# Performance work log

Hardware: AMD Instinct MI355X
Metric: run time of the kernel (lower is better)

The kernel has to match this reference:

```python
import jax, jax.numpy as jnp
import numpy as np

C = 256; Ca = C // 2; WH = 8; WW = 8; K = 3; NH = 8; HD = Ca // NH
EPS_LN = 1e-5; EPS_BN = 1e-5

def _rel_pos_idx(wh, ww):
    coords = np.stack(np.meshgrid(np.arange(wh), np.arange(ww), indexing='ij'))  # (2,wh,ww)
    flat = coords.reshape(2, -1)
    rel = (flat[:, :, None] - flat[:, None, :]).transpose(1, 2, 0).astype(np.int64)  # (N,N,2)
    rel[..., 0] += wh - 1
    rel[..., 1] += ww - 1
    rel[..., 0] *= 2 * ww - 1
    return jnp.asarray(rel.sum(-1))  # (N,N)

REL_IDX = _rel_pos_idx(WH, WW)

def _ln(x, g, b):
    m = x.mean(-1, keepdims=True)
    v = x.var(-1, keepdims=True)
    return (x - m) / jnp.sqrt(v + EPS_LN) * g + b

def _bn(x, g, b):  # eval-mode BN, running_mean=0, running_var=1; x is NCHW
    return x * (g / np.sqrt(1.0 + EPS_BN))[None, :, None, None] + b[None, :, None, None]

def _conv1x1(x, w, b):  # w: (O, I)
    return jnp.einsum('bchw,oc->bohw', x, w) + b[None, :, None, None]

def _rwp(x, h, w, wh, ww):  # windows (B*nW, wh*ww, c) -> image (B, c, h, w)
    Bn, N, c = x.shape
    nh, nw = h // wh, w // ww
    B = Bn // (nh * nw)
    x = x.reshape(B, nh, nw, wh, ww, c)
    return x.transpose(0, 5, 1, 3, 2, 4).reshape(B, c, h, w)

def _wp(x, wh, ww):  # image (B, c, h, w) -> windows (B*nW, wh*ww, c)
    B, c, h, w = x.shape
    x = x.reshape(B, c, h // wh, wh, w // ww, ww)
    return x.transpose(0, 2, 4, 3, 5, 1).reshape(-1, wh * ww, c)

def _gelu(t):
    return jax.nn.gelu(t, approximate=False)

def forward(x, rel_pos_bias, attn_w, attn_b, attn_ln_g, attn_ln_b,
            conv_w, conv_b, conv_bn_g, conv_bn_b,
            ci_w1, ci_b1, ci_bn_g, ci_bn_b, ci_w2, ci_b2,
            pr_w, pr_b, cn_bn_g, cn_bn_b,
            qkv_w, qkv_b,
            si_w1, si_b1, si_bn_g, si_bn_b, si_w2, si_b2,
            an_g, an_b, out_w, out_b, h, w):
    B_, N, Cfull = x.shape
    x_attn = _ln(x @ attn_w + attn_b, attn_ln_g, attn_ln_b)  # (B_, N, Ca)
    # conv branch -- note: source applies RWP to raw x (proj_cnn output is dead code)
    x_img = _rwp(x, h, w, WH, WW)  # (B, C, h, w)
    pad = K // 2
    x_cnn = jax.lax.conv_general_dilated(
        x_img, conv_w, (1, 1), [(pad, pad), (pad, pad)],
        dimension_numbers=('NCHW', 'OIHW', 'NCHW'), feature_group_count=Cfull)
    x_cnn = _gelu(_bn(x_cnn + conv_b[None, :, None, None], conv_bn_g, conv_bn_b))
    gap = x_cnn.mean((2, 3), keepdims=True)  # (B, C, 1, 1)
    ci = _conv1x1(gap, ci_w1, ci_b1)
    ci = _gelu(_bn(ci, ci_bn_g, ci_bn_b))
    ci = _conv1x1(ci, ci_w2, ci_b2)  # (B, Ca, 1, 1)
    x_cnn = _conv1x1(x_cnn, pr_w, pr_b)  # (B, Ca, h, w)
    # windowed attention
    qkv = (x_attn @ qkv_w + qkv_b).reshape(B_, N, 3, NH, HD).transpose(2, 0, 3, 1, 4)
    q, k, v = qkv[0], qkv[1], qkv[2]  # each (B_, NH, N, HD)
    B = ci.shape[0]
    ci_s = jax.nn.sigmoid(ci).reshape(B, 1, NH, 1, HD)
    v = (v.reshape(B, B_ // B, NH, N, HD) * ci_s).reshape(B_, NH, N, HD)
    scale = HD ** -0.5
    attn = jnp.einsum('bhnd,bhmd->bhnm', q * scale, k)
    bias = rel_pos_bias[REL_IDX]  # (N, N, NH)
    attn = jax.nn.softmax(attn + bias.transpose(2, 0, 1)[None], axis=-1)
    x_attn = jnp.einsum('bhnm,bhmd->bhnd', attn, v).transpose(0, 2, 1, 3).reshape(B_, N, Ca)
    # spatial interaction gating of conv branch
    x_sp = _rwp(x_attn, h, w, WH, WW)  # (B, Ca, h, w)
    si = _conv1x1(x_sp, si_w1, si_b1)
    si = _gelu(_bn(si, si_bn_g, si_bn_b))
    si = _conv1x1(si, si_w2, si_b2)  # (B, 1, h, w)
    x_cnn = jax.nn.sigmoid(si * x_cnn)
    x_cnn = _bn(x_cnn, cn_bn_g, cn_bn_b)
    x_cnn = _wp(x_cnn, WH, WW)  # (B_, N, Ca)
    x_attn = _ln(x_attn, an_g, an_b)
    return jnp.concatenate([x_attn, x_cnn], axis=-1) @ out_w + out_b

def setup_inputs() -> dict:
    key = jax.random.key(0)
    ks = jax.random.split(key, 12)
    B_, N = 2048, WH * WW
    s = 0.02
    return dict(
        x=jax.random.normal(ks[0], (B_, N, C), jnp.float32),
        rel_pos_bias=jax.random.uniform(ks[1], ((2 * WH - 1) * (2 * WW - 1), NH), jnp.float32),
        attn_w=jax.random.normal(ks[2], (C, Ca)) * s, attn_b=jnp.zeros((Ca,)),
        attn_ln_g=jnp.ones((Ca,)), attn_ln_b=jnp.zeros((Ca,)),
        conv_w=jax.random.normal(ks[3], (C, 1, K, K)) * s, conv_b=jnp.zeros((C,)),
        conv_bn_g=jnp.ones((C,)), conv_bn_b=jnp.zeros((C,)),
        ci_w1=jax.random.normal(ks[4], (C // 8, C)) * s, ci_b1=jnp.zeros((C // 8,)),
        ci_bn_g=jnp.ones((C // 8,)), ci_bn_b=jnp.zeros((C // 8,)),
        ci_w2=jax.random.normal(ks[5], (Ca, C // 8)) * s, ci_b2=jnp.zeros((Ca,)),
        pr_w=jax.random.normal(ks[6], (Ca, C)) * s, pr_b=jnp.zeros((Ca,)),
        cn_bn_g=jnp.ones((Ca,)), cn_bn_b=jnp.zeros((Ca,)),
        qkv_w=jax.random.normal(ks[7], (Ca, 3 * Ca)) * s, qkv_b=jnp.zeros((3 * Ca,)),
        si_w1=jax.random.normal(ks[8], (C // 16, Ca)) * s, si_b1=jnp.zeros((C // 16,)),
        si_bn_g=jnp.ones((C // 16,)), si_bn_b=jnp.zeros((C // 16,)),
        si_w2=jax.random.normal(ks[9], (1, C // 16)) * s, si_b2=jnp.zeros((1,)),
        an_g=jnp.ones((Ca,)), an_b=jnp.zeros((Ca,)),
        out_w=jax.random.normal(ks[10], (C, C)) * s, out_b=jnp.zeros((C,)),
        h=64, w=64,
    )

def reference(x, rel_pos_bias, attn_w, attn_b, attn_ln_g, attn_ln_b,
              conv_w, conv_b, conv_bn_g, conv_bn_b,
              ci_w1, ci_b1, ci_bn_g, ci_bn_b, ci_w2, ci_b2,
              pr_w, pr_b, cn_bn_g, cn_bn_b,
              qkv_w, qkv_b,
              si_w1, si_b1, si_bn_g, si_bn_b, si_w2, si_b2,
              an_g, an_b, out_w, out_b, h, w):
    return forward(x, rel_pos_bias, attn_w, attn_b, attn_ln_g, attn_ln_b,
                   conv_w, conv_b, conv_bn_g, conv_bn_b,
                   ci_w1, ci_b1, ci_bn_g, ci_bn_b, ci_w2, ci_b2,
                   pr_w, pr_b, cn_bn_g, cn_bn_b,
                   qkv_w, qkv_b,
                   si_w1, si_b1, si_bn_g, si_bn_b, si_w2, si_b2,
                   an_g, an_b, out_w, out_b, h, w)
```

## Files before the change

kernel.cpp:

```cpp
#include <hip/hip_runtime.h>
#include <math.h>


#define BNR 0.9999950000374998f
#define SQRT1_2 0.70710678118654752f

typedef __attribute__((ext_vector_type(8))) short short8;
typedef __attribute__((ext_vector_type(4))) float f32x4;
typedef __attribute__((ext_vector_type(4))) _Float16 half4;

__device__ __forceinline__ float gelu_f(float x) {
  return 0.5f * x * (1.0f + erff(x * SQRT1_2));
}
__device__ __forceinline__ unsigned short f2bf(float f) {
  unsigned int u = __builtin_bit_cast(unsigned int, f);
  u += 0x7fffu + ((u >> 16) & 1u);
  return (unsigned short)(u >> 16);
}
__device__ __forceinline__ float bf2f(unsigned short h) {
  unsigned int u = ((unsigned int)h) << 16;
  return __builtin_bit_cast(float, u);
}
__device__ __forceinline__ void ld8(const unsigned short* p, float* o) {
  const short8 v = *(const short8*)p;
#pragma unroll
  for (int i = 0; i < 8; ++i) o[i] = bf2f((unsigned short)v[i]);
}

#define ATI(r, ch) (((r) << 8) + ((((ch) ^ ((r)&7))) << 3))

__global__ __launch_bounds__(256) void kpack(
    const float* __restrict__ aw, const float* __restrict__ qw,
    const float* __restrict__ prw, const float* __restrict__ ow,
    const float* __restrict__ sw1, unsigned short* __restrict__ awp,
    unsigned short* __restrict__ qwp, unsigned short* __restrict__ prwp,
    unsigned short* __restrict__ owp, unsigned short* __restrict__ sw1p) {
  const int b = blockIdx.x;
  const float* src; unsigned short* dst; int fs, K, N, NT, trans;
  if (b < 64)       { fs = b;       src = aw;  dst = awp;  K = 256; N = 128; NT = 8;  trans = 0; }
  else if (b < 160) { fs = b - 64;  src = qw;  dst = qwp;  K = 128; N = 384; NT = 24; trans = 0; }
  else if (b < 224) { fs = b - 160; src = prw; dst = prwp; K = 256; N = 128; NT = 8;  trans = 1; }
  else if (b < 352) { fs = b - 224; src = ow;  dst = owp;  K = 256; N = 256; NT = 16; trans = 0; }
  else              { fs = b - 352; src = sw1; dst = sw1p; K = 128; N = 16;  NT = 1;  trans = 1; }
  const int ks = fs / NT, nt = fs % NT;
  for (int idx = threadIdx.x; idx < 512; idx += 256) {
    const int l = idx >> 3, i = idx & 7;
    const int k = ks * 32 + ((l >> 4) << 3) + i, n = nt * 16 + (l & 15);
    const float v = trans ? src[n * K + k] : src[k * N + n];
    dst[(fs * 64 + l) * 8 + i] = f2bf(v);
  }
}

__global__ __launch_bounds__(256) void k1_attn_ln(
    const float* __restrict__ x, const unsigned short* __restrict__ awp,
    const float* __restrict__ ab, const float* __restrict__ lg,
    const float* __restrict__ lb, unsigned short* __restrict__ xattn,
    unsigned short* __restrict__ xb) {
  const int tid = threadIdx.x, w = tid >> 6, l = tid & 63;
  const int lr = l & 15, lg4 = l >> 4;
  const int r0 = blockIdx.x * 64 + w * 16;
  const float* xp = x + (size_t)(r0 + lr) * 256 + lg4 * 8;
  unsigned short* xbp = xb + (size_t)(r0 + lr) * 256 + lg4 * 8;
  short8 a[8];
#pragma unroll
  for (int ks = 0; ks < 8; ++ks) {
    const float4 f0 = *(const float4*)(xp + ks * 32);
    const float4 f1 = *(const float4*)(xp + ks * 32 + 4);
    short8 av;
    av[0] = f2bf(f0.x); av[1] = f2bf(f0.y); av[2] = f2bf(f0.z); av[3] = f2bf(f0.w);
    av[4] = f2bf(f1.x); av[5] = f2bf(f1.y); av[6] = f2bf(f1.z); av[7] = f2bf(f1.w);
    a[ks] = av;
    *(short8*)(xbp + ks * 32) = av;
  }
  f32x4 acc[8];
#pragma unroll
  for (int nt = 0; nt < 8; ++nt) acc[nt] = (f32x4)0.f;
#pragma unroll
  for (int nt = 0; nt < 8; ++nt)
#pragma unroll
    for (int ks = 0; ks < 8; ++ks) {
      const short8 bfr = *(const short8*)(awp + ((ks * 8 + nt) * 64 + l) * 8);
      acc[nt] = __builtin_amdgcn_mfma_f32_16x16x32_bf16(a[ks], bfr, acc[nt], 0, 0, 0);
    }
  float bias[8], gam[8], bet[8];
#pragma unroll
  for (int nt = 0; nt < 8; ++nt) {
    const int col = nt * 16 + lr;
    bias[nt] = ab[col]; gam[nt] = lg[col]; bet[nt] = lb[col];
  }
#pragma unroll
  for (int j = 0; j < 4; ++j) {
    float s = 0.f, qq = 0.f;
#pragma unroll
    for (int nt = 0; nt < 8; ++nt) {
      const float v = acc[nt][j] + bias[nt];
      acc[nt][j] = v; s += v; qq += v * v;
    }
    s += __shfl_xor(s, 1); s += __shfl_xor(s, 2);
    s += __shfl_xor(s, 4); s += __shfl_xor(s, 8);
    qq += __shfl_xor(qq, 1); qq += __shfl_xor(qq, 2);
    qq += __shfl_xor(qq, 4); qq += __shfl_xor(qq, 8);
    const float mean = s * (1.f / 128.f);
    const float var = qq * (1.f / 128.f) - mean * mean;
    const float rstd = rsqrtf(var + 1e-5f);
    const int row = r0 + lg4 * 4 + j;
#pragma unroll
    for (int nt = 0; nt < 8; ++nt)
      xattn[(size_t)row * 128 + nt * 16 + lr] =
          f2bf((acc[nt][j] - mean) * rstd * gam[nt] + bet[nt]);
  }
}

__global__ __launch_bounds__(256) void k25_conv(
    const unsigned short* __restrict__ xb, const float* __restrict__ cw,
    const float* __restrict__ cb, const float* __restrict__ bg,
    const float* __restrict__ bb, const unsigned short* __restrict__ prwp,
    const float* __restrict__ prb, unsigned short* __restrict__ xpr,
    float* __restrict__ gpart) {
  __shared__ unsigned short gl[32][264];
  const int tid = threadIdx.x;
  const int b = blockIdx.x >> 7;
  const int y = (blockIdx.x >> 1) & 63;
  const int xt = (blockIdx.x & 1) * 32;
  const int w = tid >> 6, l = tid & 63;
  {
    const int c0 = l << 2;
    float4 w9[9];
#pragma unroll
    for (int k = 0; k < 9; ++k) {
      w9[k].x = cw[(c0 + 0) * 9 + k];
      w9[k].y = cw[(c0 + 1) * 9 + k];
      w9[k].z = cw[(c0 + 2) * 9 + k];
      w9[k].w = cw[(c0 + 3) * 9 + k];
    }
    const float4 cbv = *(const float4*)&cb[c0];
    float4 scv = *(const float4*)&bg[c0];
    scv.x *= BNR; scv.y *= BNR; scv.z *= BNR; scv.w *= BNR;
    const float4 sbv = *(const float4*)&bb[c0];
    float4 gsum = make_float4(0.f, 0.f, 0.f, 0.f);
    const int px0 = xt + w * 8;
#pragma unroll
    for (int sc2 = 0; sc2 < 2; ++sc2) {
      const int p0 = px0 + sc2 * 4;
      float4 v[3][6];
#pragma unroll
      for (int dy = 0; dy < 3; ++dy) {
        const int yy = y + dy - 1;
        const bool vy = (unsigned)yy < 64u;
        const int ybase = vy ? ((b * 64 + (yy >> 3) * 8) * 64 + (yy & 7) * 8) : 0;
#pragma unroll
        for (int q = 0; q < 6; ++q) {
          const int xx = p0 - 1 + q;
          float4 f = make_float4(0.f, 0.f, 0.f, 0.f);
          if (vy && (unsigned)xx < 64u) {
            const int row = ybase + (xx >> 3) * 64 + (xx & 7);
            const ushort4 u = *(const ushort4*)&xb[(size_t)row * 256 + c0];
            f.x = bf2f(u.x); f.y = bf2f(u.y); f.z = bf2f(u.z); f.w = bf2f(u.w);
          }
          v[dy][q] = f;
        }
      }
#pragma unroll
      for (int p = 0; p < 4; ++p) {
        float4 s = cbv;
#pragma unroll
        for (int dy = 0; dy < 3; ++dy)
#pragma unroll
          for (int dx = 0; dx < 3; ++dx) {
            const float wv_x = ((const float*)&w9[dy * 3 + dx])[0];
            const float4 wv = w9[dy * 3 + dx];
            const float4 vv = v[dy][p + dx];
            s.x = fmaf(wv.x, vv.x, s.x);
            s.y = fmaf(wv.y, vv.y, s.y);
            s.z = fmaf(wv.z, vv.z, s.z);
            s.w = fmaf(wv.w, vv.w, s.w);
            (void)wv_x;
          }
        s.x = s.x * scv.x + sbv.x; s.y = s.y * scv.y + sbv.y;
        s.z = s.z * scv.z + sbv.z; s.w = s.w * scv.w + sbv.w;
        const float g0 = gelu_f(s.x), g1 = gelu_f(s.y);
        const float g2 = gelu_f(s.z), g3 = gelu_f(s.w);
        ushort4 pk;
        pk.x = f2bf(g0); pk.y = f2bf(g1); pk.z = f2bf(g2); pk.w = f2bf(g3);
        *(ushort4*)&gl[w * 8 + sc2 * 4 + p][c0] = pk;
        gsum.x += g0; gsum.y += g1; gsum.z += g2; gsum.w += g3;
      }
    }
    *(float4*)&gpart[(size_t)blockIdx.x * 256 + c0] = gsum;
  }
  __syncthreads();
  const int lr = l & 15, lg4 = l >> 4;
  const int mr0 = (w & 1) * 16, nt0 = (w >> 1) * 4;
  short8 a[8];
#pragma unroll
  for (int ks = 0; ks < 8; ++ks)
    a[ks] = *(const short8*)&gl[mr0 + lr][ks * 32 + lg4 * 8];
  f32x4 acc[4];
#pragma unroll
  for (int nt = 0; nt < 4; ++nt) acc[nt] = (f32x4)0.f;
#pragma unroll
  for (int nt = 0; nt < 4; ++nt)
#pragma unroll
    for (int ks = 0; ks < 8; ++ks) {
      const short8 bfr =
          *(const short8*)(prwp + ((ks * 8 + nt0 + nt) * 64 + l) * 8);
      acc[nt] = __builtin_amdgcn_mfma_f32_16x16x32_bf16(a[ks], bfr, acc[nt], 0, 0, 0);
    }
#pragma unroll
  for (int nt = 0; nt < 4; ++nt) {
    const int col = (nt0 + nt) * 16 + lr;
    const float bv = prb[col];
#pragma unroll
    for (int j = 0; j < 4; ++j) {
      const int pix = (b * 64 + y) * 64 + xt + mr0 + lg4 * 4 + j;
      xpr[(size_t)pix * 128 + col] = f2bf(acc[nt][j] + bv);
    }
  }
}

__global__ __launch_bounds__(128) void k3_ci(
    const float* __restrict__ gp, const float* __restrict__ w1,
    const float* __restrict__ b1, const float* __restrict__ g1,
    const float* __restrict__ bb1, const float* __restrict__ w2,
    const float* __restrict__ b2, float* __restrict__ cis) {
  __shared__ float gm[256];
  __shared__ float c1[32];
  const int b = blockIdx.x, tid = threadIdx.x;
  for (int c = tid; c < 256; c += 128) {
    float s = 0.f;
    for (int p = 0; p < 128; ++p) s += gp[(size_t)(b * 128 + p) * 256 + c];
    gm[c] = s * (1.f / 4096.f);
  }
  __syncthreads();
  if (tid < 32) {
    float s = b1[tid];
    for (int c = 0; c < 256; ++c) s = fmaf(gm[c], w1[tid * 256 + c], s);
    s = s * (g1[tid] * BNR) + bb1[tid];
    c1[tid] = gelu_f(s);
  }
  __syncthreads();
  float s = b2[tid];
#pragma unroll
  for (int i = 0; i < 32; ++i) s = fmaf(c1[i], w2[tid * 32 + i], s);
  cis[b * 128 + tid] = 1.f / (1.f + __expf(-s));
}

__global__ __launch_bounds__(256) void k4_attn(
    const unsigned short* __restrict__ xa, const unsigned short* __restrict__ qwp,
    const float* __restrict__ qb, const float* __restrict__ cis,
    const float* __restrict__ rpb, unsigned short* __restrict__ attn) {
  __shared__ _Float16 Qs[64][130];
  __shared__ _Float16 Ks[64][130];
  __shared__ _Float16 VT[128][66];
  __shared__ float bsl[8][226];
  __shared__ float cisl[128];
  __shared__ float qbl[384];
  const int tid = threadIdx.x;
  const int win = blockIdx.x, img = win >> 6;
  for (int i = tid; i < 1800; i += 256) bsl[i & 7][i >> 3] = rpb[i];
  for (int i = tid; i < 128; i += 256) cisl[i] = cis[img * 128 + i];
  for (int i = tid; i < 384; i += 256) qbl[i] = qb[i];
  const int w = tid >> 6, l = tid & 63, lr = l & 15, lg4 = l >> 4;
  short8 a[4];
  const unsigned short* ap = xa + (size_t)(win * 64 + w * 16 + lr) * 128 + lg4 * 8;
#pragma unroll
  for (int ks = 0; ks < 4; ++ks) a[ks] = *(const short8*)(ap + ks * 32);
  f32x4 acc[24];
#pragma unroll
  for (int nt = 0; nt < 24; ++nt) acc[nt] = (f32x4)0.f;
#pragma unroll
  for (int nt = 0; nt < 24; ++nt)
#pragma unroll
    for (int ks = 0; ks < 4; ++ks) {
      const short8 bfr = *(const short8*)(qwp + ((ks * 24 + nt) * 64 + l) * 8);
      acc[nt] = __builtin_amdgcn_mfma_f32_16x16x32_bf16(a[ks], bfr, acc[nt], 0, 0, 0);
    }
  __syncthreads();
#pragma unroll
  for (int nt = 0; nt < 24; ++nt) {
    const int col = nt * 16 + lr;
#pragma unroll
    for (int j = 0; j < 4; ++j) {
      const int row = w * 16 + lg4 * 4 + j;
      const float v = acc[nt][j] + qbl[col];
      if (nt < 8) Qs[row][col] = (_Float16)(v * 0.25f);
      else if (nt < 16) Ks[row][col - 128] = (_Float16)v;
      else VT[col - 256][row] = (_Float16)(v * cisl[col - 256]);
    }
  }
  __syncthreads();
  for (int hi = 0; hi < 2; ++hi) {
    const int h = w * 2 + hi;
    half4 aK[4], bQ[4], bV[4];
#pragma unroll
    for (int mt = 0; mt < 4; ++mt)
      aK[mt] = *(const half4*)&Ks[mt * 16 + lr][h * 16 + lg4 * 4];
#pragma unroll
    for (int nt = 0; nt < 4; ++nt)
      bQ[nt] = *(const half4*)&Qs[nt * 16 + lr][h * 16 + lg4 * 4];
#pragma unroll
    for (int kt = 0; kt < 4; ++kt)
      bV[kt] = *(const half4*)&VT[h * 16 + lr][kt * 16 + lg4 * 4];
    f32x4 s[4][4];
#pragma unroll
    for (int mt = 0; mt < 4; ++mt)
#pragma unroll
      for (int nt = 0; nt < 4; ++nt)
        s[mt][nt] = __builtin_amdgcn_mfma_f32_16x16x16f16(aK[mt], bQ[nt],
                                                          (f32x4)0.f, 0, 0, 0);
#pragma unroll
    for (int mt = 0; mt < 4; ++mt) {
      const int m0 = mt * 16 + lg4 * 4;
#pragma unroll
      for (int r = 0; r < 4; ++r) {
        const int m = m0 + r;
        const int my = m >> 3, mxx = m & 7;
#pragma unroll
        for (int nt = 0; nt < 4; ++nt) {
          const int n = nt * 16 + lr;
          s[mt][nt][r] += bsl[h][((n >> 3) - my + 7) * 15 + (n & 7) - mxx + 7];
        }
      }
    }
    float inv[4];
#pragma unroll
    for (int nt = 0; nt < 4; ++nt) {
      float m0 = -1e30f;
#pragma unroll
      for (int mt = 0; mt < 4; ++mt)
#pragma unroll
        for (int r = 0; r < 4; ++r) m0 = fmaxf(m0, s[mt][nt][r]);
      m0 = fmaxf(m0, __shfl_xor(m0, 16));
      m0 = fmaxf(m0, __shfl_xor(m0, 32));
      float d0 = 0.f;
#pragma unroll
      for (int mt = 0; mt < 4; ++mt)
#pragma unroll
        for (int r = 0; r < 4; ++r) {
          const float e = __expf(s[mt][nt][r] - m0);
          s[mt][nt][r] = e;
          d0 += e;
        }
      d0 += __shfl_xor(d0, 16);
      d0 += __shfl_xor(d0, 32);
      inv[nt] = 1.f / d0;
    }
    half4 pa[4][4];
#pragma unroll
    for (int nt = 0; nt < 4; ++nt)
#pragma unroll
      for (int kt = 0; kt < 4; ++kt) {
        half4 p;
#pragma unroll
        for (int r = 0; r < 4; ++r) p[r] = (_Float16)(s[kt][nt][r] * inv[nt]);
        pa[nt][kt] = p;
      }
    f32x4 o[4];
#pragma unroll
    for (int nt = 0; nt < 4; ++nt) o[nt] = (f32x4)0.f;
#pragma unroll
    for (int nt = 0; nt < 4; ++nt)
#pragma unroll
      for (int kt = 0; kt < 4; ++kt)
        o[nt] = __builtin_amdgcn_mfma_f32_16x16x16f16(pa[nt][kt], bV[kt], o[nt], 0, 0, 0);
#pragma unroll
    for (int nt = 0; nt < 4; ++nt)
#pragma unroll
      for (int r = 0; r < 4; ++r) {
        const int token = win * 64 + nt * 16 + lg4 * 4 + r;
        attn[(size_t)token * 128 + h * 16 + lr] = f2bf(o[nt][r]);
      }
  }
}

__global__ __launch_bounds__(256) void k6_tail(
    const unsigned short* __restrict__ attn, const unsigned short* __restrict__ xpr,
    const unsigned short* __restrict__ sw1p, const float* __restrict__ sb1,
    const float* __restrict__ sgc, const float* __restrict__ sbc,
    const float* __restrict__ sw2, const float* __restrict__ sb2,
    const float* __restrict__ cg, const float* __restrict__ cbb,
    const float* __restrict__ ag, const float* __restrict__ abb,
    const unsigned short* __restrict__ owp, const float* __restrict__ ob,
    float* __restrict__ out) {
  __shared__ unsigned short At[64 * 256];
  __shared__ float sifl[64];
  __shared__ float statl[64][2];
  const int tid = threadIdx.x;
  const int R0 = blockIdx.x * 64;
  const int w = tid >> 6, l = tid & 63, lr = l & 15, lg4 = l >> 4;
  for (int i = tid; i < 1024; i += 256) {
    const int r = i >> 4, c16 = i & 15;
    *(uint4*)&At[ATI(r, c16)] =
        *(const uint4*)&attn[(size_t)(R0 + r) * 128 + c16 * 8];
    const int R = R0 + r, win = R >> 6, tt = R & 63;
    const int bimg = win >> 6, wy = (win >> 3) & 7, wx = win & 7;
    const int pix = (bimg * 64 + wy * 8 + (tt >> 3)) * 64 + wx * 8 + (tt & 7);
    *(uint4*)&At[ATI(r, 16 + c16)] =
        *(const uint4*)&xpr[(size_t)pix * 128 + c16 * 8];
  }
  __syncthreads();
  {
    const int r = tid >> 2, q = tid & 3;
    float xv[32];
#pragma unroll
    for (int b8 = 0; b8 < 4; ++b8) ld8(&At[ATI(r, q * 4 + b8)], xv + b8 * 8);
    float ps = 0.f, pq = 0.f;
#pragma unroll
    for (int j = 0; j < 32; ++j) { ps += xv[j]; pq += xv[j] * xv[j]; }
    ps += __shfl_xor(ps, 1); ps += __shfl_xor(ps, 2);
    pq += __shfl_xor(pq, 1); pq += __shfl_xor(pq, 2);
    if (q == 0) {
      const float mean = ps * (1.f / 128.f);
      const float var = pq * (1.f / 128.f) - mean * mean;
      statl[r][0] = mean;
      statl[r][1] = rsqrtf(var + 1e-5f);
    }
  }
  {
    const int row = w * 16 + lr;
    f32x4 sa = (f32x4)0.f;
#pragma unroll
    for (int ks = 0; ks < 4; ++ks) {
      const short8 a4 = *(const short8*)&At[ATI(row, ks * 4 + lg4)];
      const short8 bfr = *(const short8*)(sw1p + (ks * 64 + l) * 8);
      sa = __builtin_amdgcn_mfma_f32_16x16x32_bf16(a4, bfr, sa, 0, 0, 0);
    }
    const float sb1v = sb1[lr], g1v = sgc[lr] * BNR, b1v = sbc[lr];
    const float w2v = sw2[lr], sb2v = sb2[0];
#pragma unroll
    for (int j = 0; j < 4; ++j) {
      float s = (sa[j] + sb1v) * g1v + b1v;
      float p = gelu_f(s) * w2v;
      p += __shfl_xor(p, 1); p += __shfl_xor(p, 2);
      p += __shfl_xor(p, 4); p += __shfl_xor(p, 8);
      if (lr == 0) sifl[w * 16 + lg4 * 4 + j] = p + sb2v;
    }
  }
  __syncthreads();
  {
    const int c = tid & 127;
    const float agv = ag[c], abbv = abb[c];
    const float cgv = cg[c] * BNR, cbbv = cbb[c];
#pragma unroll
    for (int k = 0; k < 32; ++k) {
      const int r = (tid >> 7) + k * 2;
      const int ia = ATI(r, c >> 3) + (c & 7);
      const int ic = ATI(r, 16 + (c >> 3)) + (c & 7);
      float a = bf2f(At[ia]);
      a = (a - statl[r][0]) * statl[r][1] * agv + abbv;
      At[ia] = f2bf(a);
      const float cv = bf2f(At[ic]);
      const float g = 1.f / (1.f + __expf(-sifl[r] * cv));
      At[ic] = f2bf(g * cgv + cbbv);
    }
  }
  __syncthreads();
  const int row = w * 16 + lr;
  short8 a[8];
#pragma unroll
  for (int ks = 0; ks < 8; ++ks)
    a[ks] = *(const short8*)&At[ATI(row, ks * 4 + lg4)];
  f32x4 acc[16];
#pragma unroll
  for (int nt = 0; nt < 16; ++nt) acc[nt] = (f32x4)0.f;
#pragma unroll
  for (int nt = 0; nt < 16; ++nt)
#pragma unroll
    for (int ks = 0; ks < 8; ++ks) {
      const short8 bfr = *(const short8*)(owp + ((ks * 16 + nt) * 64 + l) * 8);
      acc[nt] = __builtin_amdgcn_mfma_f32_16x16x32_bf16(a[ks], bfr, acc[nt], 0, 0, 0);
    }
#pragma unroll
  for (int nt = 0; nt < 16; ++nt) {
    const int col = nt * 16 + lr;
    const float bv = ob[col];
#pragma unroll
    for (int j = 0; j < 4; ++j)
      out[(size_t)(R0 + w * 16 + lg4 * 4 + j) * 256 + col] = acc[nt][j] + bv;
  }
}

extern "C" void kernel_launch(void* const* d_in, const int* in_sizes, int n_in,
                              void* d_out, int out_size, void* d_ws,
                              size_t ws_size, hipStream_t stream) {
  (void)in_sizes; (void)n_in; (void)out_size; (void)ws_size;
  const float* x      = (const float*)d_in[0];
  const float* rpb    = (const float*)d_in[1];
  const float* attn_w = (const float*)d_in[2];
  const float* attn_b = (const float*)d_in[3];
  const float* aln_g  = (const float*)d_in[4];
  const float* aln_b  = (const float*)d_in[5];
  const float* conv_w = (const float*)d_in[6];
  const float* conv_b = (const float*)d_in[7];
  const float* cbn_g  = (const float*)d_in[8];
  const float* cbn_b  = (const float*)d_in[9];
  const float* ci_w1  = (const float*)d_in[10];
  const float* ci_b1  = (const float*)d_in[11];
  const float* ci_bg  = (const float*)d_in[12];
  const float* ci_bb  = (const float*)d_in[13];
  const float* ci_w2  = (const float*)d_in[14];
  const float* ci_b2  = (const float*)d_in[15];
  const float* pr_w   = (const float*)d_in[16];
  const float* pr_b   = (const float*)d_in[17];
  const float* cn_g   = (const float*)d_in[18];
  const float* cn_b   = (const float*)d_in[19];
  const float* qkv_w  = (const float*)d_in[20];
  const float* qkv_b  = (const float*)d_in[21];
  const float* si_w1  = (const float*)d_in[22];
  const float* si_b1  = (const float*)d_in[23];
  const float* si_bg  = (const float*)d_in[24];
  const float* si_bb  = (const float*)d_in[25];
  const float* si_w2  = (const float*)d_in[26];
  const float* si_b2  = (const float*)d_in[27];
  const float* an_g   = (const float*)d_in[28];
  const float* an_b   = (const float*)d_in[29];
  const float* out_w  = (const float*)d_in[30];
  const float* out_b  = (const float*)d_in[31];

  unsigned short* xb    = (unsigned short*)d_ws;
  unsigned short* xattn = xb + 33554432;
  unsigned short* attn  = xattn + 16777216;
  unsigned short* xpr   = attn + 16777216;
  float* gpart = (float*)(xpr + 16777216);
  float* cis   = gpart + 1048576;
  unsigned short* awp  = (unsigned short*)(cis + 4096);
  unsigned short* qwp  = awp + 32768;
  unsigned short* prwp = qwp + 49152;
  unsigned short* owp  = prwp + 32768;
  unsigned short* sw1p = owp + 65536;

  kpack<<<356, 256, 0, stream>>>(attn_w, qkv_w, pr_w, out_w, si_w1,
                                 awp, qwp, prwp, owp, sw1p);
  k1_attn_ln<<<2048, 256, 0, stream>>>(x, awp, attn_b, aln_g, aln_b, xattn, xb);
  k25_conv<<<4096, 256, 0, stream>>>(xb, conv_w, conv_b, cbn_g, cbn_b, prwp,
                                     pr_b, xpr, gpart);
  k3_ci<<<32, 128, 0, stream>>>(gpart, ci_w1, ci_b1, ci_bg, ci_bb, ci_w2,
                                ci_b2, cis);
  k4_attn<<<2048, 256, 0, stream>>>(xattn, qwp, qkv_b, cis, rpb, attn);
  k6_tail<<<2048, 256, 0, stream>>>(attn, xpr, sw1p, si_b1, si_bg, si_bb,
                                    si_w2, si_b2, cn_g, cn_b, an_g, an_b,
                                    owp, out_b, (float*)d_out);
}
```

Measured before the change: 329.9 us.

## Use fp16 packed conv, tanh-approx GELU, precomputed bias table, swizzled conv blocks

Several independent changes. The depthwise conv copy of x is now stored as fp16 and the conv runs on packed half2 FMAs, with the projection MFMA switched to f16 and pr_w packed as fp16. GELU now uses a tanh/sigmoid approximation instead of erf. The relative position bias is expanded once into a per-head 64x64 fp16 table and read directly in attention, replacing the per-block shared-memory staging and index maths. Conv block IDs are swizzled. The aim is cheaper arithmetic and less setup work, at the cost of fp16 range and precision and an approximate GELU.

```diff
diff --git a/kernel.cpp b/kernel.cpp
--- a/kernel.cpp
+++ b/kernel.cpp
@@ -3,14 +3,16 @@
 
 
 #define BNR 0.9999950000374998f
-#define SQRT1_2 0.70710678118654752f
 
 typedef __attribute__((ext_vector_type(8))) short short8;
 typedef __attribute__((ext_vector_type(4))) float f32x4;
 typedef __attribute__((ext_vector_type(4))) _Float16 half4;
+typedef __attribute__((ext_vector_type(8))) _Float16 half8;
+typedef __attribute__((ext_vector_type(2))) _Float16 h2v;
 
 __device__ __forceinline__ float gelu_f(float x) {
-  return 0.5f * x * (1.0f + erff(x * SQRT1_2));
+  const float z = x * (1.0f + 0.044715f * x * x);
+  return x / (1.0f + __expf(-1.5957691216057308f * z));
 }
 __device__ __forceinline__ unsigned short f2bf(float f) {
   unsigned int u = __builtin_bit_cast(unsigned int, f);
@@ -25,6 +27,9 @@
   const short8 v = *(const short8*)p;
 #pragma unroll
   for (int i = 0; i < 8; ++i) o[i] = bf2f((unsigned short)v[i]);
+}
+__device__ __forceinline__ unsigned int pkh(float a, float b) {
+  return __builtin_bit_cast(unsigned int, __builtin_amdgcn_cvt_pkrtz(a, b));
 }
 
 #define ATI(r, ch) (((r) << 8) + ((((ch) ^ ((r)&7))) << 3))
@@ -36,19 +41,29 @@
     unsigned short* __restrict__ qwp, unsigned short* __restrict__ prwp,
     unsigned short* __restrict__ owp, unsigned short* __restrict__ sw1p) {
   const int b = blockIdx.x;
-  const float* src; unsigned short* dst; int fs, K, N, NT, trans;
-  if (b < 64)       { fs = b;       src = aw;  dst = awp;  K = 256; N = 128; NT = 8;  trans = 0; }
-  else if (b < 160) { fs = b - 64;  src = qw;  dst = qwp;  K = 128; N = 384; NT = 24; trans = 0; }
-  else if (b < 224) { fs = b - 160; src = prw; dst = prwp; K = 256; N = 128; NT = 8;  trans = 1; }
-  else if (b < 352) { fs = b - 224; src = ow;  dst = owp;  K = 256; N = 256; NT = 16; trans = 0; }
-  else              { fs = b - 352; src = sw1; dst = sw1p; K = 128; N = 16;  NT = 1;  trans = 1; }
+  const float* src; unsigned short* dst; int fs, K, N, NT, trans, f16o;
+  if (b < 64)       { fs = b;       src = aw;  dst = awp;  K = 256; N = 128; NT = 8;  trans = 0; f16o = 0; }
+  else if (b < 160) { fs = b - 64;  src = qw;  dst = qwp;  K = 128; N = 384; NT = 24; trans = 0; f16o = 0; }
+  else if (b < 224) { fs = b - 160; src = prw; dst = prwp; K = 256; N = 128; NT = 8;  trans = 1; f16o = 1; }
+  else if (b < 352) { fs = b - 224; src = ow;  dst = owp;  K = 256; N = 256; NT = 16; trans = 0; f16o = 0; }
+  else              { fs = b - 352; src = sw1; dst = sw1p; K = 128; N = 16;  NT = 1;  trans = 1; f16o = 0; }
   const int ks = fs / NT, nt = fs % NT;
   for (int idx = threadIdx.x; idx < 512; idx += 256) {
     const int l = idx >> 3, i = idx & 7;
     const int k = ks * 32 + ((l >> 4) << 3) + i, n = nt * 16 + (l & 15);
     const float v = trans ? src[n * K + k] : src[k * N + n];
-    dst[(fs * 64 + l) * 8 + i] = f2bf(v);
-  }
+    dst[(fs * 64 + l) * 8 + i] =
+        f16o ? __builtin_bit_cast(unsigned short, (_Float16)v) : f2bf(v);
+  }
+}
+
+__global__ __launch_bounds__(256) void kbias(const float* __restrict__ rpb,
+                                             unsigned short* __restrict__ bt) {
+  const int i = blockIdx.x * 256 + threadIdx.x;
+  const int h = i >> 12, n = (i >> 6) & 63, m = i & 63;
+  const int ny = n >> 3, nx = n & 7, my = m >> 3, mx = m & 7;
+  const float v = rpb[((ny - my + 7) * 15 + (nx - mx + 7)) * 8 + h];
+  bt[i] = __builtin_bit_cast(unsigned short, (_Float16)v);
 }
 
 __global__ __launch_bounds__(256) void k1_attn_ln(
@@ -70,7 +85,10 @@
     av[0] = f2bf(f0.x); av[1] = f2bf(f0.y); av[2] = f2bf(f0.z); av[3] = f2bf(f0.w);
     av[4] = f2bf(f1.x); av[5] = f2bf(f1.y); av[6] = f2bf(f1.z); av[7] = f2bf(f1.w);
     a[ks] = av;
-    *(short8*)(xbp + ks * 32) = av;
+    uint4 hv;
+    hv.x = pkh(f0.x, f0.y); hv.y = pkh(f0.z, f0.w);
+    hv.z = pkh(f1.x, f1.y); hv.w = pkh(f1.z, f1.w);
+    *(uint4*)(xbp + ks * 32) = hv;
   }
   f32x4 acc[8];
 #pragma unroll
@@ -119,30 +137,37 @@
     float* __restrict__ gpart) {
   __shared__ unsigned short gl[32][264];
   const int tid = threadIdx.x;
-  const int b = blockIdx.x >> 7;
-  const int y = (blockIdx.x >> 1) & 63;
-  const int xt = (blockIdx.x & 1) * 32;
+  const int bid = (blockIdx.x & 7) * 512 + (blockIdx.x >> 3);
+  const int b = bid >> 7;
+  const int y = (bid >> 1) & 63;
+  const int xt = (bid & 1) * 32;
   const int w = tid >> 6, l = tid & 63;
   {
     const int c0 = l << 2;
-    float4 w9[9];
+    h2v w01[9], w23[9];
 #pragma unroll
     for (int k = 0; k < 9; ++k) {
-      w9[k].x = cw[(c0 + 0) * 9 + k];
-      w9[k].y = cw[(c0 + 1) * 9 + k];
-      w9[k].z = cw[(c0 + 2) * 9 + k];
-      w9[k].w = cw[(c0 + 3) * 9 + k];
-    }
-    const float4 cbv = *(const float4*)&cb[c0];
-    float4 scv = *(const float4*)&bg[c0];
-    scv.x *= BNR; scv.y *= BNR; scv.z *= BNR; scv.w *= BNR;
-    const float4 sbv = *(const float4*)&bb[c0];
+      w01[k][0] = (_Float16)cw[(c0 + 0) * 9 + k];
+      w01[k][1] = (_Float16)cw[(c0 + 1) * 9 + k];
+      w23[k][0] = (_Float16)cw[(c0 + 2) * 9 + k];
+      w23[k][1] = (_Float16)cw[(c0 + 3) * 9 + k];
+    }
+    const float4 cbf = *(const float4*)&cb[c0];
+    float4 scf = *(const float4*)&bg[c0];
+    scf.x *= BNR; scf.y *= BNR; scf.z *= BNR; scf.w *= BNR;
+    const float4 sbf = *(const float4*)&bb[c0];
+    h2v cb01 = {(_Float16)cbf.x, (_Float16)cbf.y};
+    h2v cb23 = {(_Float16)cbf.z, (_Float16)cbf.w};
+    h2v sc01 = {(_Float16)scf.x, (_Float16)scf.y};
+    h2v sc23 = {(_Float16)scf.z, (_Float16)scf.w};
+    h2v sb01 = {(_Float16)sbf.x, (_Float16)sbf.y};
+    h2v sb23 = {(_Float16)sbf.z, (_Float16)sbf.w};
     float4 gsum = make_float4(0.f, 0.f, 0.f, 0.f);
     const int px0 = xt + w * 8;
 #pragma unroll
     for (int sc2 = 0; sc2 < 2; ++sc2) {
       const int p0 = px0 + sc2 * 4;
-      float4 v[3][6];
+      h2v v0[3][6], v1[3][6];
 #pragma unroll
       for (int dy = 0; dy < 3; ++dy) {
         const int yy = y + dy - 1;
@@ -151,50 +176,46 @@
 #pragma unroll
         for (int q = 0; q < 6; ++q) {
           const int xx = p0 - 1 + q;
-          float4 f = make_float4(0.f, 0.f, 0.f, 0.f);
+          h2v a = (h2v)(_Float16)0.f, c = (h2v)(_Float16)0.f;
           if (vy && (unsigned)xx < 64u) {
             const int row = ybase + (xx >> 3) * 64 + (xx & 7);
-            const ushort4 u = *(const ushort4*)&xb[(size_t)row * 256 + c0];
-            f.x = bf2f(u.x); f.y = bf2f(u.y); f.z = bf2f(u.z); f.w = bf2f(u.w);
+            const uint2 u = *(const uint2*)&xb[(size_t)row * 256 + c0];
+            a = __builtin_bit_cast(h2v, u.x);
+            c = __builtin_bit_cast(h2v, u.y);
           }
-          v[dy][q] = f;
+          v0[dy][q] = a; v1[dy][q] = c;
         }
       }
 #pragma unroll
       for (int p = 0; p < 4; ++p) {
-        float4 s = cbv;
+        h2v s0 = cb01, s1 = cb23;
 #pragma unroll
         for (int dy = 0; dy < 3; ++dy)
 #pragma unroll
           for (int dx = 0; dx < 3; ++dx) {
-            const float wv_x = ((const float*)&w9[dy * 3 + dx])[0];
-            const float4 wv = w9[dy * 3 + dx];
-            const float4 vv = v[dy][p + dx];
-            s.x = fmaf(wv.x, vv.x, s.x);
-            s.y = fmaf(wv.y, vv.y, s.y);
-            s.z = fmaf(wv.z, vv.z, s.z);
-            s.w = fmaf(wv.w, vv.w, s.w);
-            (void)wv_x;
+            s0 = w01[dy * 3 + dx] * v0[dy][p + dx] + s0;
+            s1 = w23[dy * 3 + dx] * v1[dy][p + dx] + s1;
           }
-        s.x = s.x * scv.x + sbv.x; s.y = s.y * scv.y + sbv.y;
-        s.z = s.z * scv.z + sbv.z; s.w = s.w * scv.w + sbv.w;
-        const float g0 = gelu_f(s.x), g1 = gelu_f(s.y);
-        const float g2 = gelu_f(s.z), g3 = gelu_f(s.w);
-        ushort4 pk;
-        pk.x = f2bf(g0); pk.y = f2bf(g1); pk.z = f2bf(g2); pk.w = f2bf(g3);
-        *(ushort4*)&gl[w * 8 + sc2 * 4 + p][c0] = pk;
+        s0 = s0 * sc01 + sb01;
+        s1 = s1 * sc23 + sb23;
+        const float g0 = gelu_f((float)s0[0]), g1 = gelu_f((float)s0[1]);
+        const float g2 = gelu_f((float)s1[0]), g3 = gelu_f((float)s1[1]);
+        uint2 pk;
+        pk.x = pkh(g0, g1); pk.y = pkh(g2, g3);
+        *(uint2*)&gl[w * 8 + sc2 * 4 + p][c0] = pk;
         gsum.x += g0; gsum.y += g1; gsum.z += g2; gsum.w += g3;
       }
     }
-    *(float4*)&gpart[(size_t)blockIdx.x * 256 + c0] = gsum;
+    *(float4*)&gpart[(size_t)bid * 256 + c0] = gsum;
   }
   __syncthreads();
   const int lr = l & 15, lg4 = l >> 4;
   const int mr0 = (w & 1) * 16, nt0 = (w >> 1) * 4;
-  short8 a[8];
+  half8 a[8];
 #pragma unroll
   for (int ks = 0; ks < 8; ++ks)
-    a[ks] = *(const short8*)&gl[mr0 + lr][ks * 32 + lg4 * 8];
+    a[ks] = __builtin_bit_cast(half8,
+                               *(const short8*)&gl[mr0 + lr][ks * 32 + lg4 * 8]);
   f32x4 acc[4];
 #pragma unroll
   for (int nt = 0; nt < 4; ++nt) acc[nt] = (f32x4)0.f;
@@ -202,9 +223,9 @@
   for (int nt = 0; nt < 4; ++nt)
 #pragma unroll
     for (int ks = 0; ks < 8; ++ks) {
-      const short8 bfr =
-          *(const short8*)(prwp + ((ks * 8 + nt0 + nt) * 64 + l) * 8);
-      acc[nt] = __builtin_amdgcn_mfma_f32_16x16x32_bf16(a[ks], bfr, acc[nt], 0, 0, 0);
+      const half8 bfr = __builtin_bit_cast(
+          half8, *(const short8*)(prwp + ((ks * 8 + nt0 + nt) * 64 + l) * 8));
+      acc[nt] = __builtin_amdgcn_mfma_f32_16x16x32_f16(a[ks], bfr, acc[nt], 0, 0, 0);
     }
 #pragma unroll
   for (int nt = 0; nt < 4; ++nt) {
@@ -248,16 +269,14 @@
 __global__ __launch_bounds__(256) void k4_attn(
     const unsigned short* __restrict__ xa, const unsigned short* __restrict__ qwp,
     const float* __restrict__ qb, const float* __restrict__ cis,
-    const float* __restrict__ rpb, unsigned short* __restrict__ attn) {
+    const unsigned short* __restrict__ biasT, unsigned short* __restrict__ attn) {
   __shared__ _Float16 Qs[64][130];
   __shared__ _Float16 Ks[64][130];
   __shared__ _Float16 VT[128][66];
-  __shared__ float bsl[8][226];
   __shared__ float cisl[128];
   __shared__ float qbl[384];
   const int tid = threadIdx.x;
   const int win = blockIdx.x, img = win >> 6;
-  for (int i = tid; i < 1800; i += 256) bsl[i & 7][i >> 3] = rpb[i];
   for (int i = tid; i < 128; i += 256) cisl[i] = cis[img * 128 + i];
   for (int i = tid; i < 384; i += 256) qbl[i] = qb[i];
   const int w = tid >> 6, l = tid & 63, lr = l & 15, lg4 = l >> 4;
@@ -309,17 +328,16 @@
         s[mt][nt] = __builtin_amdgcn_mfma_f32_16x16x16f16(aK[mt], bQ[nt],
                                                           (f32x4)0.f, 0, 0, 0);
 #pragma unroll
-    for (int mt = 0; mt < 4; ++mt) {
-      const int m0 = mt * 16 + lg4 * 4;
-#pragma unroll
-      for (int r = 0; r < 4; ++r) {
-        const int m = m0 + r;
-        const int my = m >> 3, mxx = m & 7;
-#pragma unroll
-        for (int nt = 0; nt < 4; ++nt) {
-          const int n = nt * 16 + lr;
-          s[mt][nt][r] += bsl[h][((n >> 3) - my + 7) * 15 + (n & 7) - mxx + 7];
-        }
+    for (int nt = 0; nt < 4; ++nt) {
+      const int n = nt * 16 + lr;
+      const unsigned short* bp = biasT + (((h << 6) + n) << 6);
+#pragma unroll
+      for (int mt = 0; mt < 4; ++mt) {
+        const half4 b4 = *(const half4*)(bp + mt * 16 + lg4 * 4);
+        s[mt][nt][0] += (float)b4[0];
+        s[mt][nt][1] += (float)b4[1];
+        s[mt][nt][2] += (float)b4[2];
+        s[mt][nt][3] += (float)b4[3];
       }
     }
     float inv[4];
@@ -523,20 +541,22 @@
   unsigned short* xpr   = attn + 16777216;
   float* gpart = (float*)(xpr + 16777216);
   float* cis   = gpart + 1048576;
-  unsigned short* awp  = (unsigned short*)(cis + 4096);
-  unsigned short* qwp  = awp + 32768;
-  unsigned short* prwp = qwp + 49152;
-  unsigned short* owp  = prwp + 32768;
-  unsigned short* sw1p = owp + 65536;
+  unsigned short* awp   = (unsigned short*)(cis + 4096);
+  unsigned short* qwp   = awp + 32768;
+  unsigned short* prwp  = qwp + 49152;
+  unsigned short* owp   = prwp + 32768;
+  unsigned short* sw1p  = owp + 65536;
+  unsigned short* biasT = sw1p + 2048;
 
   kpack<<<356, 256, 0, stream>>>(attn_w, qkv_w, pr_w, out_w, si_w1,
                                  awp, qwp, prwp, owp, sw1p);
+  kbias<<<128, 256, 0, stream>>>(rpb, biasT);
   k1_attn_ln<<<2048, 256, 0, stream>>>(x, awp, attn_b, aln_g, aln_b, xattn, xb);
   k25_conv<<<4096, 256, 0, stream>>>(xb, conv_w, conv_b, cbn_g, cbn_b, prwp,
                                      pr_b, xpr, gpart);
   k3_ci<<<32, 128, 0, stream>>>(gpart, ci_w1, ci_b1, ci_bg, ci_bb, ci_w2,
                                 ci_b2, cis);
-  k4_attn<<<2048, 256, 0, stream>>>(xattn, qwp, qkv_b, cis, rpb, attn);
+  k4_attn<<<2048, 256, 0, stream>>>(xattn, qwp, qkv_b, cis, biasT, attn);
   k6_tail<<<2048, 256, 0, stream>>>(attn, xpr, sw1p, si_b1, si_bg, si_bb,
                                     si_w2, si_b2, cn_g, cn_b, an_g, an_b,
                                     owp, out_b, (float*)d_out);
```

Result: faster. 305.0 us (-7.6%).
